# Performance work log

Hardware: AMD Instinct MI355X
Metric: run time of the kernel (lower is better)

Reference implementation:

```python
import jax, jax.numpy as jnp
import numpy as np

NUM_ITERATIONS = 3


def squash(s):
    # s: [..., out_channels]; norm over last axis (matches torch squash on squeezed tensor)
    norm = jnp.linalg.norm(s, axis=-1, keepdims=True)
    return (norm ** 2 / (1.0 + norm ** 2)) * (s / norm)


def setup_inputs() -> dict:
    key = jax.random.key(0)
    k1, k2 = jax.random.split(key)
    B, R, C, O, I = 256, 192, 96, 16, 20
    x = jax.random.normal(k1, (B, R, I), dtype=jnp.float32)
    W = jax.random.normal(k2, (R, C, O, I), dtype=jnp.float32)
    return {"x": x, "W": W}


def reference(x, W):
    # u_hat[b,r,c,o] = W[r,c,o,i] @ x[b,r,i]  (torch: matmul(W, x[i]) per batch element)
    u_hat = jnp.einsum('rcoi,bri->brco', W, x)  # [B,R,C,O]
    R, C = W.shape[0], W.shape[1]
    b_ij = jnp.zeros((R, C), dtype=x.dtype)  # shared across batch (torch b_ij is [1,R,C,1])
    v_j = None
    for it in range(NUM_ITERATIONS):
        c_ij = jax.nn.softmax(b_ij, axis=0)                 # softmax over routes (dim=1 in torch)
        s_j = jnp.einsum('rc,brco->bco', c_ij, u_hat)        # weighted sum over routes
        v_j = squash(s_j)                                    # [B,C,O]
        if it < NUM_ITERATIONS - 1:
            # agreement: <u_hat, v_j> averaged over batch (torch mean(dim=0))
            a_ij = jnp.einsum('brco,bco->rc', u_hat, v_j) / x.shape[0]
            b_ij = b_ij + a_ij
    return v_j  # [B, num_capsules, out_channels] (torch returns trailing singleton [B,C,O,1])
```

## Files before the change

### kernel.cpp

```cpp
#include <hip/hip_runtime.h>


#define R_ 192
#define C_ 96
#define O_ 16
#define I_ 20
#define B_ 256
#define K1 3840
#define N_ 1536
#define ZSPLIT 15
#define KCH 256
#define STILE 393216

typedef unsigned short u16;
typedef __attribute__((ext_vector_type(8))) short short8;
typedef __attribute__((ext_vector_type(4))) float floatx4;

__device__ inline float bf2f(u16 h) {
  union { unsigned int u; float f; } x; x.u = ((unsigned int)h) << 16; return x.f;
}
__device__ inline u16 f2bf(float f) {
  union { float f; unsigned int u; } x; x.f = f;
  unsigned int r = x.u + 0x7FFFu + ((x.u >> 16) & 1u);
  return (u16)(r >> 16);
}
__device__ inline unsigned int pack2(float a, float b) {
  return (unsigned int)f2bf(a) | ((unsigned int)f2bf(b) << 16);
}
__device__ inline void async16(const u16* g, u16* l) {
  __builtin_amdgcn_global_load_lds(
      (__attribute__((address_space(1))) void*)(unsigned long long)g,
      (__attribute__((address_space(3))) void*)(unsigned int)(unsigned long long)l,
      16, 0, 0);
}

__global__ void k_prep(const float* __restrict__ W, const float* __restrict__ X,
                       u16* __restrict__ WtT, u16* __restrict__ Xk,
                       u16* __restrict__ xT, float* __restrict__ bij) {
  int bid = blockIdx.x;
  if (bid < 5760) {
    int r = bid / 30, xb = bid - r * 30;
    int j4 = (xb << 10) + ((int)threadIdx.x << 2);
    int c = j4 / 320, rem = j4 - c * 320;
    int o = rem / 20, i = rem - o * 20;
    float4 v = *(const float4*)(W + (size_t)r * (C_ * O_ * I_) + j4);
    ushort4 h;
    h.x = f2bf(v.x); h.y = f2bf(v.y); h.z = f2bf(v.z); h.w = f2bf(v.w);
    *(ushort4*)&WtT[(size_t)(c * O_ + o) * K1 + r * I_ + i] = h;
  } else if (bid < 6000) {
    __shared__ u16 tile[64][72];
    int idx = bid - 5760;
    int kb = (idx % 60) << 6, bb = (idx / 60) << 6;
    int brow = threadIdx.x >> 4;
    int kq = (threadIdx.x & 15) << 2;
    #pragma unroll
    for (int p = 0; p < 4; ++p) {
      int bl = p * 16 + brow;
      float4 v = *(const float4*)(X + (size_t)(bb + bl) * K1 + kb + kq);
      ushort4 h;
      h.x = f2bf(v.x); h.y = f2bf(v.y); h.z = f2bf(v.z); h.w = f2bf(v.w);
      *(ushort4*)(Xk + (size_t)(bb + bl) * K1 + kb + kq) = h;
      tile[kq + 0][bl] = h.x;
      tile[kq + 1][bl] = h.y;
      tile[kq + 2][bl] = h.z;
      tile[kq + 3][bl] = h.w;
    }
    __syncthreads();
    int kr = threadIdx.x >> 3;
    int bq = (threadIdx.x & 7) << 3;
    #pragma unroll
    for (int q = 0; q < 2; ++q) {
      int kl = q * 32 + kr;
      *(uint4*)(xT + (size_t)(kb + kl) * B_ + bb + bq) = *(const uint4*)&tile[kl][bq];
    }
  } else {
    int t = ((bid - 6000) * 256 + threadIdx.x) << 2;
    if (t < R_ * C_) *(float4*)&bij[t] = (float4){0.f, 0.f, 0.f, 0.f};
  }
}

__device__ inline uint4 scale_b8(uint4 raw, int kg, const float* smrow) {
  int r0 = kg / I_;
  int bnd = (r0 + 1) * I_ - kg;
  float s0 = smrow[r0];
  float s1 = smrow[(r0 + 1 < R_) ? r0 + 1 : R_ - 1];
  union { uint4 q; u16 h[8]; } u; u.q = raw;
  #pragma unroll
  for (int j = 0; j < 8; ++j)
    u.h[j] = f2bf(bf2f(u.h[j]) * ((j < bnd) ? s0 : s1));
  return u.q;
}


__global__ __launch_bounds__(256) void gemm1(
    const u16* __restrict__ A, const u16* __restrict__ Bt,
    const float* __restrict__ bij, u16* __restrict__ P, int doScale) {
  __shared__ u16 As[2][8192];
  __shared__ u16 Bs[2][4096];
  __shared__ float sm[4][192];
  int bid = (int)blockIdx.x;
  int g = bid & 7, s5 = bid >> 3;
  int by = g * 3 + s5 % 3;
  int s3 = s5 / 3;
  int bz = s3 % 15, bx = s3 / 15;
  int tid = threadIdx.x;
  int w = tid >> 6, lane = tid & 63;
  if (doScale) {
    int c = (by << 2) + w;
    float e0 = bij[c * R_ + lane];
    float e1 = bij[c * R_ + lane + 64];
    float e2 = bij[c * R_ + lane + 128];
    float mx = fmaxf(e0, fmaxf(e1, e2));
    #pragma unroll
    for (int off = 32; off > 0; off >>= 1) mx = fmaxf(mx, __shfl_xor(mx, off));
    e0 = expf(e0 - mx); e1 = expf(e1 - mx); e2 = expf(e2 - mx);
    float s = e0 + e1 + e2;
    #pragma unroll
    for (int off = 32; off > 0; off >>= 1) s += __shfl_xor(s, off);
    float inv = 1.0f / s;
    sm[w][lane] = e0 * inv;
    sm[w][lane + 64] = e1 * inv;
    sm[w][lane + 128] = e2 * inv;
  }

  long m0 = (long)bx * 128, n0 = (long)by * 64;
  int k0 = bz * KCH;
  const u16* Ab = A + m0 * K1 + k0;
  const u16* Bb = Bt + n0 * K1 + k0;
  int q_s = ((lane & 3) - ((lane >> 3) & 3)) & 3;
  const u16* AgC[4]; int AlC[4];
  #pragma unroll
  for (int m = 0; m < 4; ++m) {
    AgC[m] = Ab + (long)(((m & 1) << 6) + (w << 4) + (lane >> 2)) * K1
             + ((m >> 1) << 5) + (q_s << 3);
    AlC[m] = (m << 11) + (w << 9);
  }
  const u16* BgC[2]; int BlC[2];
  #pragma unroll
  for (int m = 0; m < 2; ++m) {
    BgC[m] = Bb + (long)((w << 4) + (lane >> 2)) * K1 + (m << 5) + (q_s << 3);
    BlC[m] = (m << 11) + (w << 9);
  }
  int rowD = tid >> 2;
  int qD = ((tid & 3) - ((tid >> 3) & 3)) & 3;
  const u16* Bgs = Bb + (long)rowD * K1 + (qD << 3);
  const float* smrow = &sm[w][0];
  int wm = (w >> 1) << 6, wn = (w & 1) << 5;
  int quad = lane >> 4, lrow = lane & 15;
  int swz = ((quad + (lrow >> 1)) & 3) << 3;
  floatx4 acc[4][2];
  #pragma unroll
  for (int a = 0; a < 4; ++a)
    #pragma unroll
    for (int b = 0; b < 2; ++b) acc[a][b] = (floatx4){0.f, 0.f, 0.f, 0.f};

  #pragma unroll
  for (int m = 0; m < 4; ++m) async16(AgC[m], &As[0][AlC[m]]);
  uint4 b0, b1;
  if (doScale) {
    b0 = *(const uint4*)Bgs;
    b1 = *(const uint4*)(Bgs + 32);
  } else {
    async16(BgC[0], &Bs[0][BlC[0]]);
    async16(BgC[1], &Bs[0][BlC[1]]);
  }
  __syncthreads();

  int p = 0;
  for (int kt = 0; kt < 4; ++kt) {
    if (doScale) {
      int kg = k0 + (kt << 6) + (qD << 3);
      *(uint4*)&Bs[p][tid << 3] = scale_b8(b0, kg, smrow);
      *(uint4*)&Bs[p][2048 + (tid << 3)] = scale_b8(b1, kg + 32, smrow);
      __syncthreads();
    } else if (kt > 0) {
      __syncthreads();
    }
    if (kt + 1 < 4) {
      int kk = (kt + 1) << 6;
      #pragma unroll
      for (int m = 0; m < 4; ++m) async16(AgC[m] + kk, &As[p ^ 1][AlC[m]]);
      if (doScale) {
        b0 = *(const uint4*)(Bgs + kk);
        b1 = *(const uint4*)(Bgs + kk + 32);
      } else {
        async16(BgC[0] + kk, &Bs[p ^ 1][BlC[0]]);
        async16(BgC[1] + kk, &Bs[p ^ 1][BlC[1]]);
      }
    }
    #pragma unroll
    for (int s = 0; s < 2; ++s) {
      short8 af[4], bfr[2];
      #pragma unroll
      for (int ms = 0; ms < 4; ++ms)
        af[ms] = *(const short8*)&As[p][(s << 12)
                                        + ((wm + ms * 16 + lrow) << 5) + swz];
      #pragma unroll
      for (int ns = 0; ns < 2; ++ns)
        bfr[ns] = *(const short8*)&Bs[p][(s << 11)
                                         + ((wn + ns * 16 + lrow) << 5) + swz];
      #pragma unroll
      for (int ms = 0; ms < 4; ++ms)
        #pragma unroll
        for (int ns = 0; ns < 2; ++ns)
          acc[ms][ns] = __builtin_amdgcn_mfma_f32_16x16x32_bf16(
              af[ms], bfr[ns], acc[ms][ns], 0, 0, 0);
    }
    p ^= 1;
  }
  size_t zb = (size_t)bz * (size_t)STILE;
  #pragma unroll
  for (int ms = 0; ms < 4; ++ms)
    #pragma unroll
    for (int ns = 0; ns < 2; ++ns) {
      int b = (int)m0 + wm + ms * 16 + (quad << 2);
      int n = (int)n0 + wn + ns * 16 + lrow;
      uint2 pk;
      pk.x = pack2(acc[ms][ns][0], acc[ms][ns][1]);
      pk.y = pack2(acc[ms][ns][2], acc[ms][ns][3]);
      *(uint2*)&P[zb + (size_t)n * B_ + b] = pk;
    }
}

__global__ void k_redsq(const u16* __restrict__ P, float* __restrict__ out,
                        u16* __restrict__ vT, float preScale, int last) {
  __shared__ float nsq_l[4][64];
  int c = blockIdx.x, bh = blockIdx.y;
  int lane = threadIdx.x & 63, og = threadIdx.x >> 6;
  int b = (bh << 6) + lane;
  int n0 = (c << 4) + (og << 2);
  float acc[4];
  #pragma unroll
  for (int oo = 0; oo < 4; ++oo) acc[oo] = 0.f;
  #pragma unroll
  for (int z = 0; z < ZSPLIT; ++z) {
    size_t base = (size_t)z * STILE + (size_t)n0 * B_ + b;
    #pragma unroll
    for (int oo = 0; oo < 4; ++oo)
      acc[oo] += bf2f(P[base + (size_t)oo * B_]);
  }
  #pragma unroll
  for (int oo = 0; oo < 4; ++oo) acc[oo] *= preScale;
  float q = acc[0] * acc[0] + acc[1] * acc[1] + acc[2] * acc[2] + acc[3] * acc[3];
  nsq_l[og][lane] = q;
  __syncthreads();
  float nsq = nsq_l[0][lane] + nsq_l[1][lane] + nsq_l[2][lane] + nsq_l[3][lane];
  float f = nsq / ((1.0f + nsq) * sqrtf(nsq));
  #pragma unroll
  for (int oo = 0; oo < 4; ++oo) acc[oo] *= f;
  if (last) {
    *(float4*)(out + (size_t)b * N_ + n0) = (float4){acc[0], acc[1], acc[2], acc[3]};
  } else {
    #pragma unroll
    for (int oo = 0; oo < 4; ++oo)
      vT[(size_t)(n0 + oo) * B_ + b] = f2bf(acc[oo]);
  }
}

__global__ __launch_bounds__(256) void gemm2_agree(
    const u16* __restrict__ A, const u16* __restrict__ Bt,
    const u16* __restrict__ WtT, float* __restrict__ bij) {
  const int K = 256;
  __shared__ u16 As[2][8192];
  __shared__ u16 Bs[2][4096];
  int bid = (int)blockIdx.x;
  int g = bid & 7, s5 = bid >> 3;
  int by = g * 3 + s5 % 3;
  int bx = s5 / 3;
  int tid = threadIdx.x;
  long m0 = (long)bx * 128, n0 = (long)by * 64;
  const u16* Ab = A + m0 * K;
  const u16* Bb = Bt + n0 * K;
  int w = tid >> 6, lane = tid & 63;
  int wm = (w >> 1) << 6, wn = (w & 1) << 5;
  int quad = lane >> 4, lrow = lane & 15;
  int swz = ((quad + (lrow >> 1)) & 3) << 3;
  int q_s = ((lane & 3) - ((lane >> 3) & 3)) & 3;
  const u16* AgC[4]; int AlC[4];
  #pragma unroll
  for (int m = 0; m < 4; ++m) {
    AgC[m] = Ab + (long)(((m & 1) << 6) + (w << 4) + (lane >> 2)) * K
             + ((m >> 1) << 5) + (q_s << 3);
    AlC[m] = (m << 11) + (w << 9);
  }
  const u16* BgC[2]; int BlC[2];
  #pragma unroll
  for (int m = 0; m < 2; ++m) {
    BgC[m] = Bb + (long)((w << 4) + (lane >> 2)) * K + (m << 5) + (q_s << 3);
    BlC[m] = (m << 11) + (w << 9);
  }
  floatx4 acc[4][2];
  #pragma unroll
  for (int a = 0; a < 4; ++a)
    #pragma unroll
    for (int b = 0; b < 2; ++b) acc[a][b] = (floatx4){0.f, 0.f, 0.f, 0.f};

  #pragma unroll
  for (int m = 0; m < 4; ++m) async16(AgC[m], &As[0][AlC[m]]);
  async16(BgC[0], &Bs[0][BlC[0]]);
  async16(BgC[1], &Bs[0][BlC[1]]);

  int p = 0;
  #pragma unroll
  for (int kt = 0; kt < 4; ++kt) {
    __syncthreads();
    if (kt + 1 < 4) {
      int kk = (kt + 1) << 6;
      #pragma unroll
      for (int m = 0; m < 4; ++m) async16(AgC[m] + kk, &As[p ^ 1][AlC[m]]);
      async16(BgC[0] + kk, &Bs[p ^ 1][BlC[0]]);
      async16(BgC[1] + kk, &Bs[p ^ 1][BlC[1]]);
    }
    #pragma unroll
    for (int s = 0; s < 2; ++s) {
      short8 af[4], bfr[2];
      #pragma unroll
      for (int ms = 0; ms < 4; ++ms)
        af[ms] = *(const short8*)&As[p][(s << 12)
                                        + ((wm + ms * 16 + lrow) << 5) + swz];
      #pragma unroll
      for (int ns = 0; ns < 2; ++ns)
        bfr[ns] = *(const short8*)&Bs[p][(s << 11)
                                         + ((wn + ns * 16 + lrow) << 5) + swz];
      #pragma unroll
      for (int ms = 0; ms < 4; ++ms)
        #pragma unroll
        for (int ns = 0; ns < 2; ++ns)
          acc[ms][ns] = __builtin_amdgcn_mfma_f32_16x16x32_bf16(
              af[ms], bfr[ns], acc[ms][ns], 0, 0, 0);
    }
    p ^= 1;
  }
  #pragma unroll
  for (int ms = 0; ms < 4; ++ms) {
    int rowbase = (int)m0 + wm + ms * 16;
    int r_lo = rowbase / I_;
    int r_hi = (rowbase + 15) / I_;
    int bnd = (r_lo + 1) * I_;
    int rowl = rowbase + (quad << 2);
    #pragma unroll
    for (int ns = 0; ns < 2; ++ns) {
      int col = (int)n0 + wn + ns * 16 + lrow;
      uint2 wv = *(const uint2*)&WtT[(size_t)col * K1 + rowl];
      u16 h[4];
      h[0] = (u16)(wv.x & 0xffff); h[1] = (u16)(wv.x >> 16);
      h[2] = (u16)(wv.y & 0xffff); h[3] = (u16)(wv.y >> 16);
      float p0 = 0.f, p1 = 0.f;
      #pragma unroll
      for (int e = 0; e < 4; ++e) {
        float pr = acc[ms][ns][e] * bf2f(h[e]);
        if (rowl + e < bnd) p0 += pr; else p1 += pr;
      }
      #pragma unroll
      for (int off = 32; off > 0; off >>= 1) {
        p0 += __shfl_xor(p0, off);
        p1 += __shfl_xor(p1, off);
      }
      if (lane == 0) {
        int c = col >> 4;
        atomicAdd(&bij[c * R_ + r_lo], p0 * (1.0f / 256.0f));
        atomicAdd(&bij[c * R_ + r_hi], p1 * (1.0f / 256.0f));
      }
    }
  }
}

extern "C" void kernel_launch(void* const* d_in, const int* in_sizes, int n_in,
                              void* d_out, int out_size, void* d_ws, size_t ws_size,
                              hipStream_t stream) {
  const float* X = (const float*)d_in[0];
  const float* W = (const float*)d_in[1];
  float* out = (float*)d_out;
  char* ws = (char*)d_ws;
  u16*  WtT = (u16*)(ws);
  u16*  Xk  = (u16*)(ws + 11796480);
  u16*  xT  = (u16*)(ws + 13762560);
  u16*  vT  = (u16*)(ws + 15728640);
  u16*  Pb  = (u16*)(ws + 16515072);
  float* bij = (float*)(ws + 28311552);

  k_prep<<<6018, 256, 0, stream>>>(W, X, WtT, Xk, xT, bij);

  for (int it = 0; it < 3; ++it) {
    gemm1<<<720, 256, 0, stream>>>(Xk, WtT, bij, Pb, it > 0);
    k_redsq<<<dim3(96, 4), 256, 0, stream>>>(
        Pb, out, vT, it == 0 ? (1.0f / 192.0f) : 1.0f, it == 2);
    if (it < 2)
      gemm2_agree<<<720, 256, 0, stream>>>(xT, vT, WtT, bij);
  }
}
```

Measured before the change: 147.5 us.

## Fuse split-K reduction and squash into agreement GEMM kernel per capsule

Replaces the separate k_redsq + gemm2_agree pair on the first two iterations with a single rsg2 kernel. Each block reduces the split-K partials for one capsule, applies squash into a bf16 v tile held in shared memory, then streams a strip of xT through MFMA to produce the agreement contributions. This removes one launch per iteration and the vT round-trip through global memory. The cost is that each capsule's reduction is recomputed by several M-strip blocks, the grid drops to 480 blocks, and there is a serial loop of 24 steps with small per-block MFMA tiles.

```diff
diff --git a/kernel.cpp b/kernel.cpp
--- a/kernel.cpp
+++ b/kernel.cpp
@@ -257,111 +257,136 @@
   }
 }
 
-__global__ __launch_bounds__(256) void gemm2_agree(
-    const u16* __restrict__ A, const u16* __restrict__ Bt,
-    const u16* __restrict__ WtT, float* __restrict__ bij) {
-  const int K = 256;
+__global__ __launch_bounds__(256) void rsg2(
+    const u16* __restrict__ P, const u16* __restrict__ A,
+    const u16* __restrict__ WtT, float* __restrict__ bij, float preScale) {
+  __shared__ float sv[16][258];
+  __shared__ float fl[256];
+  __shared__ u16 vB[16][264];
   __shared__ u16 As[2][8192];
-  __shared__ u16 Bs[2][4096];
   int bid = (int)blockIdx.x;
-  int g = bid & 7, s5 = bid >> 3;
-  int by = g * 3 + s5 % 3;
-  int bx = s5 / 3;
+  int g = bid & 7, s8 = bid >> 3;
+  int c = g * 12 + s8 % 12;
+  int mstrip = s8 / 12;
   int tid = threadIdx.x;
-  long m0 = (long)bx * 128, n0 = (long)by * 64;
-  const u16* Ab = A + m0 * K;
-  const u16* Bb = Bt + n0 * K;
   int w = tid >> 6, lane = tid & 63;
-  int wm = (w >> 1) << 6, wn = (w & 1) << 5;
   int quad = lane >> 4, lrow = lane & 15;
-  int swz = ((quad + (lrow >> 1)) & 3) << 3;
+
+  {
+    int o_ = tid >> 4, bg = tid & 15;
+    const u16* Pb0 = P + (size_t)((c << 4) + o_) * B_ + (bg << 3);
+    float a0[8], a1[8];
+    #pragma unroll
+    for (int j = 0; j < 8; ++j) { a0[j] = 0.f; a1[j] = 0.f; }
+    #pragma unroll
+    for (int z = 0; z < ZSPLIT; ++z) {
+      union { uint4 q; u16 h[8]; } u, v;
+      u.q = *(const uint4*)(Pb0 + (size_t)z * STILE);
+      v.q = *(const uint4*)(Pb0 + 128 + (size_t)z * STILE);
+      #pragma unroll
+      for (int j = 0; j < 8; ++j) { a0[j] += bf2f(u.h[j]); a1[j] += bf2f(v.h[j]); }
+    }
+    #pragma unroll
+    for (int j = 0; j < 8; ++j) {
+      sv[o_][(bg << 3) + j] = a0[j] * preScale;
+      sv[o_][128 + (bg << 3) + j] = a1[j] * preScale;
+    }
+    __syncthreads();
+    {
+      int b = tid;
+      float nsq = 0.f;
+      #pragma unroll
+      for (int o = 0; o < 16; ++o) { float v = sv[o][b]; nsq += v * v; }
+      fl[b] = nsq / ((1.0f + nsq) * sqrtf(nsq));
+    }
+    __syncthreads();
+    #pragma unroll
+    for (int h = 0; h < 2; ++h) {
+      int b0 = (bg << 3) + (h << 7);
+      uint4 o4; unsigned int* po = (unsigned int*)&o4;
+      #pragma unroll
+      for (int j = 0; j < 4; ++j) {
+        float lo = sv[o_][b0 + 2 * j]     * fl[b0 + 2 * j];
+        float hi = sv[o_][b0 + 2 * j + 1] * fl[b0 + 2 * j + 1];
+        po[j] = pack2(lo, hi);
+      }
+      *(uint4*)&vB[o_][b0] = o4;
+    }
+  }
+  __syncthreads();
+
+  const u16* A0 = A + (size_t)mstrip * (768 * 256);
   int q_s = ((lane & 3) - ((lane >> 3) & 3)) & 3;
-  const u16* AgC[4]; int AlC[4];
+  int AgP[4]; int AlC[4];
   #pragma unroll
   for (int m = 0; m < 4; ++m) {
-    AgC[m] = Ab + (long)(((m & 1) << 6) + (w << 4) + (lane >> 2)) * K
+    AgP[m] = (((m & 1) << 6) + (w << 4) + (lane >> 2)) * 256
              + ((m >> 1) << 5) + (q_s << 3);
     AlC[m] = (m << 11) + (w << 9);
   }
-  const u16* BgC[2]; int BlC[2];
-  #pragma unroll
-  for (int m = 0; m < 2; ++m) {
-    BgC[m] = Bb + (long)((w << 4) + (lane >> 2)) * K + (m << 5) + (q_s << 3);
-    BlC[m] = (m << 11) + (w << 9);
-  }
-  floatx4 acc[4][2];
-  #pragma unroll
-  for (int a = 0; a < 4; ++a)
-    #pragma unroll
-    for (int b = 0; b < 2; ++b) acc[a][b] = (floatx4){0.f, 0.f, 0.f, 0.f};
-
-  #pragma unroll
-  for (int m = 0; m < 4; ++m) async16(AgC[m], &As[0][AlC[m]]);
-  async16(BgC[0], &Bs[0][BlC[0]]);
-  async16(BgC[1], &Bs[0][BlC[1]]);
-
+  #pragma unroll
+  for (int m = 0; m < 4; ++m) async16(A0 + AgP[m], &As[0][AlC[m]]);
+
+  int wm = w << 5;
+  int swzA = ((quad + (lrow >> 1)) & 3) << 3;
+  floatx4 acc[2];
+  acc[0] = (floatx4){0.f, 0.f, 0.f, 0.f};
+  acc[1] = (floatx4){0.f, 0.f, 0.f, 0.f};
   int p = 0;
-  #pragma unroll
-  for (int kt = 0; kt < 4; ++kt) {
+  #pragma unroll 1
+  for (int sidx = 0; sidx < 24; ++sidx) {
     __syncthreads();
-    if (kt + 1 < 4) {
-      int kk = (kt + 1) << 6;
-      #pragma unroll
-      for (int m = 0; m < 4; ++m) async16(AgC[m] + kk, &As[p ^ 1][AlC[m]]);
-      async16(BgC[0] + kk, &Bs[p ^ 1][BlC[0]]);
-      async16(BgC[1] + kk, &Bs[p ^ 1][BlC[1]]);
-    }
+    if (sidx + 1 < 24) {
+      int nx = sidx + 1;
+      int of = ((nx >> 2) << 15) + ((nx & 3) << 6);
+      #pragma unroll
+      for (int m = 0; m < 4; ++m) async16(A0 + of + AgP[m], &As[p ^ 1][AlC[m]]);
+    }
+    int kt = sidx & 3;
     #pragma unroll
     for (int s = 0; s < 2; ++s) {
-      short8 af[4], bfr[2];
-      #pragma unroll
-      for (int ms = 0; ms < 4; ++ms)
-        af[ms] = *(const short8*)&As[p][(s << 12)
-                                        + ((wm + ms * 16 + lrow) << 5) + swz];
-      #pragma unroll
-      for (int ns = 0; ns < 2; ++ns)
-        bfr[ns] = *(const short8*)&Bs[p][(s << 11)
-                                         + ((wn + ns * 16 + lrow) << 5) + swz];
-      #pragma unroll
-      for (int ms = 0; ms < 4; ++ms)
+      int ks = (kt << 1) + s;
+      short8 bfr = *(const short8*)&vB[lrow][(ks << 5) + (quad << 3)];
+      #pragma unroll
+      for (int ms = 0; ms < 2; ++ms) {
+        short8 af = *(const short8*)&As[p][(s << 12)
+                       + ((wm + ms * 16 + lrow) << 5) + swzA];
+        acc[ms] = __builtin_amdgcn_mfma_f32_16x16x32_bf16(af, bfr, acc[ms], 0, 0, 0);
+      }
+    }
+    if (kt == 3) {
+      int row0 = mstrip * 768 + ((sidx >> 2) << 7);
+      #pragma unroll
+      for (int ms = 0; ms < 2; ++ms) {
+        int rowbase = row0 + wm + ms * 16;
+        int r_lo = rowbase / I_;
+        int r_hi = (rowbase + 15) / I_;
+        int bnd = (r_lo + 1) * I_;
+        int rowl = rowbase + (quad << 2);
+        int col = (c << 4) + lrow;
+        uint2 wv = *(const uint2*)&WtT[(size_t)col * K1 + rowl];
+        u16 hh[4];
+        hh[0] = (u16)(wv.x & 0xffff); hh[1] = (u16)(wv.x >> 16);
+        hh[2] = (u16)(wv.y & 0xffff); hh[3] = (u16)(wv.y >> 16);
+        float p0 = 0.f, p1 = 0.f;
         #pragma unroll
-        for (int ns = 0; ns < 2; ++ns)
-          acc[ms][ns] = __builtin_amdgcn_mfma_f32_16x16x32_bf16(
-              af[ms], bfr[ns], acc[ms][ns], 0, 0, 0);
+        for (int e = 0; e < 4; ++e) {
+          float pr = acc[ms][e] * bf2f(hh[e]);
+          if (rowl + e < bnd) p0 += pr; else p1 += pr;
+        }
+        #pragma unroll
+        for (int off = 32; off > 0; off >>= 1) {
+          p0 += __shfl_xor(p0, off);
+          p1 += __shfl_xor(p1, off);
+        }
+        if (lane == 0) {
+          atomicAdd(&bij[c * R_ + r_lo], p0 * (1.0f / 256.0f));
+          atomicAdd(&bij[c * R_ + r_hi], p1 * (1.0f / 256.0f));
+        }
+        acc[ms] = (floatx4){0.f, 0.f, 0.f, 0.f};
+      }
     }
     p ^= 1;
-  }
-  #pragma unroll
-  for (int ms = 0; ms < 4; ++ms) {
-    int rowbase = (int)m0 + wm + ms * 16;
-    int r_lo = rowbase / I_;
-    int r_hi = (rowbase + 15) / I_;
-    int bnd = (r_lo + 1) * I_;
-    int rowl = rowbase + (quad << 2);
-    #pragma unroll
-    for (int ns = 0; ns < 2; ++ns) {
-      int col = (int)n0 + wn + ns * 16 + lrow;
-      uint2 wv = *(const uint2*)&WtT[(size_t)col * K1 + rowl];
-      u16 h[4];
-      h[0] = (u16)(wv.x & 0xffff); h[1] = (u16)(wv.x >> 16);
-      h[2] = (u16)(wv.y & 0xffff); h[3] = (u16)(wv.y >> 16);
-      float p0 = 0.f, p1 = 0.f;
-      #pragma unroll
-      for (int e = 0; e < 4; ++e) {
-        float pr = acc[ms][ns][e] * bf2f(h[e]);
-        if (rowl + e < bnd) p0 += pr; else p1 += pr;
-      }
-      #pragma unroll
-      for (int off = 32; off > 0; off >>= 1) {
-        p0 += __shfl_xor(p0, off);
-        p1 += __shfl_xor(p1, off);
-      }
-      if (lane == 0) {
-        int c = col >> 4;
-        atomicAdd(&bij[c * R_ + r_lo], p0 * (1.0f / 256.0f));
-        atomicAdd(&bij[c * R_ + r_hi], p1 * (1.0f / 256.0f));
-      }
-    }
   }
 }
 
@@ -381,11 +406,10 @@
 
   k_prep<<<6018, 256, 0, stream>>>(W, X, WtT, Xk, xT, bij);
 
-  for (int it = 0; it < 3; ++it) {
-    gemm1<<<720, 256, 0, stream>>>(Xk, WtT, bij, Pb, it > 0);
-    k_redsq<<<dim3(96, 4), 256, 0, stream>>>(
-        Pb, out, vT, it == 0 ? (1.0f / 192.0f) : 1.0f, it == 2);
-    if (it < 2)
-      gemm2_agree<<<720, 256, 0, stream>>>(xT, vT, WtT, bij);
-  }
-}
+  gemm1<<<720, 256, 0, stream>>>(Xk, WtT, bij, Pb, 0);
+  rsg2<<<480, 256, 0, stream>>>(Pb, xT, WtT, bij, 1.0f / 192.0f);
+  gemm1<<<720, 256, 0, stream>>>(Xk, WtT, bij, Pb, 1);
+  rsg2<<<480, 256, 0, stream>>>(Pb, xT, WtT, bij, 1.0f);
+  gemm1<<<720, 256, 0, stream>>>(Xk, WtT, bij, Pb, 1);
+  k_redsq<<<dim3(96, 4), 256, 0, stream>>>(Pb, out, vT, 1.0f, 1);
+}
```

Result: slower. 170.7 us (+15.7%).
